# Performance work log

Hardware: AMD Instinct MI355X
Metric: run time of the kernel (lower is better)

Reference implementation:

```python
import jax, jax.numpy as jnp
import numpy as np
from math import ceil

B, T, FQ, D = 2, 48, 100, 512
H, DFF, L, WSZ = 8, 2048, 6, 8


def setup_inputs() -> dict:
    key = jax.random.key(0)
    ks = jax.random.split(key, 8)
    g = lambda k, shape: jax.random.normal(k, shape, jnp.float32) * 0.02
    return {
        "frame_queries": jax.random.normal(ks[0], (B, T, FQ, D), jnp.float32),
        "Wp": g(ks[1], (D, D)), "bp": jnp.zeros((D,), jnp.float32),
        "Wqkv": g(ks[2], (L, 3 * D, D)), "bqkv": jnp.zeros((L, 3 * D), jnp.float32),
        "Wo": g(ks[3], (L, D, D)), "bo": jnp.zeros((L, D), jnp.float32),
        "ln1_s": jnp.ones((L, D), jnp.float32), "ln1_b": jnp.zeros((L, D), jnp.float32),
        "W1": g(ks[4], (L, DFF, D)), "b1": jnp.zeros((L, DFF), jnp.float32),
        "W2": g(ks[5], (L, D, DFF)), "b2": jnp.zeros((L, D), jnp.float32),
        "ln2_s": jnp.ones((L, D), jnp.float32), "ln2_b": jnp.zeros((L, D), jnp.float32),
    }


def _ln(x, s, b, eps=1e-5):
    mu = x.mean(-1, keepdims=True)
    var = ((x - mu) ** 2).mean(-1, keepdims=True)
    return (x - mu) * jax.lax.rsqrt(var + eps) * s + b


def _mha(x, Wqkv_i, bqkv_i, Wo_i, bo_i, add_mask):
    # x: [Bw, S, C]; add_mask: None or [Bw, 1, S, S] additive float
    Bw, S, C = x.shape
    hd = C // H
    qkv = x @ Wqkv_i.T + bqkv_i
    q, k, v = jnp.split(qkv, 3, axis=-1)
    q = q.reshape(Bw, S, H, hd).transpose(0, 2, 1, 3)
    k = k.reshape(Bw, S, H, hd).transpose(0, 2, 1, 3)
    v = v.reshape(Bw, S, H, hd).transpose(0, 2, 1, 3)
    scores = jnp.einsum('bhqd,bhkd->bhqk', q, k) * jnp.float32(1.0 / np.sqrt(hd))
    if add_mask is not None:
        scores = scores + add_mask
    a = jax.nn.softmax(scores, axis=-1)
    o = jnp.einsum('bhqk,bhkd->bhqd', a, v).transpose(0, 2, 1, 3).reshape(Bw, S, C)
    return o @ Wo_i.T + bo_i


def _shift_mask():
    # padding mask is all-False (T % WSZ == 0), faithful construction of the
    # shifted-window additive mask as in the torch code.
    Nw = T // WSZ
    half = int(ceil(WSZ / 2))
    S = WSZ * FQ
    am = jnp.zeros((B, T), dtype=bool)
    r = jnp.roll(am, half, axis=1).reshape(B, Nw, WSZ)
    m = jnp.broadcast_to(r[..., None], (B, Nw, WSZ, WSZ))
    m = m.at[:, 0].set(m[:, 0] | m[:, 0].swapaxes(-1, -2))
    m = m.at[:, -1].set(m[:, -1] | m[:, -1].swapaxes(-1, -2))
    m = m.at[:, 0, :half, half:].set(True)
    m = m.at[:, 0, half:, :half].set(True)
    mfull = jnp.broadcast_to(m.reshape(B * Nw, WSZ, 1, WSZ, 1),
                             (B * Nw, WSZ, FQ, WSZ, FQ)).reshape(B * Nw, S, S)
    return (mfull.astype(jnp.float32) * -1000.0)[:, None]  # [B*Nw,1,S,S]


def reference(frame_queries, Wp, bp, Wqkv, bqkv, Wo, bo, ln1_s, ln1_b,
              W1, b1, W2, b2, ln2_s, ln2_b):
    Nw = T // WSZ
    half = int(ceil(WSZ / 2))
    S = WSZ * FQ
    x = frame_queries @ Wp.T + bp  # [B, T, FQ, D]
    shift_add = _shift_mask()
    for i in range(L):
        if i % 2 == 0:
            # plain window attention
            xw = x.reshape(B * Nw, S, D)
            xw = _ln(xw + _mha(xw, Wqkv[i], bqkv[i], Wo[i], bo[i], None),
                     ln1_s[i], ln1_b[i])
            x = xw.reshape(B, T, FQ, D)
        else:
            # shifted window attention
            xs = jnp.roll(x, half, axis=1)
            xw = xs.reshape(B * Nw, S, D)
            xw = _ln(xw + _mha(xw, Wqkv[i], bqkv[i], Wo[i], bo[i], shift_add),
                     ln1_s[i], ln1_b[i])
            x = jnp.roll(xw.reshape(B, T, FQ, D), -half, axis=1)
        # FFN (pointwise over channel dim)
        h = jax.nn.relu(x @ W1[i].T + b1[i]) @ W2[i].T + b2[i]
        x = _ln(x + h, ln2_s[i], ln2_b[i])
    return x  # [B, T, FQ, D] == 'lb t nq c'
```

## Files before the change

### kernel.cpp

```cpp
#include <hip/hip_runtime.h>


typedef float  f4    __attribute__((ext_vector_type(4)));
typedef __bf16 bf8   __attribute__((ext_vector_type(8)));
typedef unsigned short u16x8 __attribute__((ext_vector_type(8)));
typedef unsigned short u16x4 __attribute__((ext_vector_type(4)));

__device__ __forceinline__ unsigned short f2bf(float f) {
    unsigned int u = __builtin_bit_cast(unsigned int, f);
    u += 0x7fffu + ((u >> 16) & 1u);
    return (unsigned short)(u >> 16);
}
__device__ __forceinline__ float bf2f(unsigned short s) {
    return __builtin_bit_cast(float, ((unsigned int)s) << 16);
}

#define GLD16(gp, lp) __builtin_amdgcn_global_load_lds( \
    (const __attribute__((address_space(1))) void*)(gp), \
    (__attribute__((address_space(3))) void*)(lp), 16, 0, 0)

__device__ __forceinline__ int map_row(int r, int rshift) {
    if (!rshift) return r;
    int bb = r / 4800, rem = r % 4800;
    int tt = rem / 100, f = rem - tt * 100;
    return bb * 4800 + ((tt + rshift) % 48) * 100 + f;
}

template<int BM>
__global__ __launch_bounds__(256) void mfma_gemm(
    const unsigned short* __restrict__ A, const unsigned short* __restrict__ W,
    const float* __restrict__ bias, float* Cf, unsigned short* Cb,
    int M, int N, int K, int relu, int rshift, int qscale, int NB, int nsplit)
{
    constexpr int MI      = BM / 32;
    constexpr int ABUF    = BM * 32;
    constexpr int SB      = ABUF + 4096;
    constexpr int AROUNDS = BM / 64;
    __shared__ unsigned short Ls[3 * SB];
    const int tid = threadIdx.x, lane = tid & 63, wave = tid >> 6;

    const int per = gridDim.x >> 3;
    const int l = (blockIdx.x & 7) * per + (blockIdx.x >> 3);
    const int MB = M / BM;
    if (l >= NB * MB * nsplit) return;
    const int sk = l / (NB * MB);
    const int l2 = l - sk * NB * MB;
    const int n0 = (l2 % NB) * 128, m0 = (l2 / NB) * BM;
    const int Ksp = K / nsplit;
    const int kbeg = sk * Ksp;

    const unsigned short* ga[AROUNDS];
    #pragma unroll
    for (int it = 0; it < AROUNDS; ++it) {
        int s = it * 256 + tid, row = s >> 2, cg = (s & 3) ^ ((row >> 1) & 3);
        ga[it] = A + (size_t)map_row(m0 + row, rshift) * K + kbeg + cg * 8;
    }
    const unsigned short* gb[2];
    #pragma unroll
    for (int it = 0; it < 2; ++it) {
        int s = it * 256 + tid, row = s >> 2, cg = (s & 3) ^ ((row >> 1) & 3);
        gb[it] = W + (size_t)(n0 + row) * K + kbeg + cg * 8;
    }

    const int wm = (wave >> 1) * (BM / 2), wn = (wave & 1) * 64;
    const int lr = lane & 15, quad = lane >> 4;

    auto STAGE = [&](int kt2, int buf) {
        const int k1 = kt2 << 5;
        unsigned short* Lb = &Ls[buf * SB];
        #pragma unroll
        for (int it = 0; it < AROUNDS; ++it)
            GLD16(ga[it] + k1, &Lb[(it * 256 + wave * 64) * 8]);
        #pragma unroll
        for (int it = 0; it < 2; ++it)
            GLD16(gb[it] + k1, &Lb[ABUF + (it * 256 + wave * 64) * 8]);
    };

    f4 acc[MI][4];
    #pragma unroll
    for (int i = 0; i < MI; ++i)
        #pragma unroll
        for (int j = 0; j < 4; ++j) acc[i][j] = 0.f;

    const int NK = Ksp >> 5;
    STAGE(0, 0);
    STAGE(1, 1);

    int cb = 0;
    for (int kt = 0; kt < NK; ++kt) {
        if (kt + 1 < NK) {
            if constexpr (BM == 128) asm volatile("s_waitcnt vmcnt(4)" ::: "memory");
            else                     asm volatile("s_waitcnt vmcnt(3)" ::: "memory");
        } else {
            asm volatile("s_waitcnt vmcnt(0)" ::: "memory");
        }
        __builtin_amdgcn_s_barrier();
        __builtin_amdgcn_sched_barrier(0);
        const int ib = (cb == 0) ? 2 : cb - 1;
        if (kt + 2 < NK) STAGE(kt + 2, ib);

        const unsigned short* Ab = &Ls[cb * SB];
        const unsigned short* Bb = &Ls[cb * SB + ABUF];
        bf8 af[MI], bfr[4];
        #pragma unroll
        for (int mi = 0; mi < MI; ++mi) {
            int m = wm + mi * 16 + lr;
            int c = quad ^ ((m >> 1) & 3);
            af[mi] = __builtin_bit_cast(bf8, *(const u16x8*)&Ab[(m * 4 + c) * 8]);
        }
        #pragma unroll
        for (int ni = 0; ni < 4; ++ni) {
            int n = wn + ni * 16 + lr;
            int c = quad ^ ((n >> 1) & 3);
            bfr[ni] = __builtin_bit_cast(bf8, *(const u16x8*)&Bb[(n * 4 + c) * 8]);
        }
        #pragma unroll
        for (int mi = 0; mi < MI; ++mi)
            #pragma unroll
            for (int ni = 0; ni < 4; ++ni)
                acc[mi][ni] = __builtin_amdgcn_mfma_f32_16x16x32_bf16(
                    af[mi], bfr[ni], acc[mi][ni], 0, 0, 0);
        __builtin_amdgcn_sched_barrier(0);
        cb = (cb + 1 == 3) ? 0 : cb + 1;
    }

    float* Cfo = Cf ? Cf + (size_t)sk * M * N : nullptr;
    unsigned short* Cbo = Cb ? Cb + (size_t)sk * M * N : nullptr;
    #pragma unroll
    for (int mi = 0; mi < MI; ++mi) {
        #pragma unroll
        for (int ni = 0; ni < 4; ++ni) {
            const int rowg = m0 + wm + mi * 16 + quad * 4;
            const int colg = n0 + wn + ni * 16 + lr;
            const float bv = (sk == 0) ? bias[colg] : 0.f;
            const float sc = (qscale && colg < 512) ? 0.125f : 1.0f;
            #pragma unroll
            for (int r = 0; r < 4; ++r) {
                float v = (acc[mi][ni][r] + bv) * sc;
                if (relu) v = fmaxf(v, 0.f);
                const size_t off = (size_t)(rowg + r) * N + colg;
                if (Cfo) Cfo[off] = v;
                if (Cbo) Cbo[off] = f2bf(v);
            }
        }
    }
}

__global__ __launch_bounds__(320) void flash_attn_mfma(
    const unsigned short* __restrict__ qkv, unsigned short* __restrict__ o,
    int masked)
{
    __shared__ unsigned short Ks[2][2048];
    __shared__ unsigned short VT[2][64 * 34];
    __shared__ unsigned short Ps[5][576];

    const int bid = blockIdx.x;
    const int h = bid & 7, kk2 = bid >> 3;
    const int qt = kk2 % 10, w = kk2 / 10;
    const int tid = threadIdx.x, lane = tid & 63, wave = tid >> 6;
    const int lr = lane & 15, quad = lane >> 4;
    const int qb = qt * 80 + wave * 16;
    const size_t wbase = (size_t)w * 800 * 1536;
    const bool do_mask = masked && ((w % 6) == 0);

    bf8 aQ[2];
    {
        const unsigned short* qp =
            qkv + wbase + (size_t)(qb + lr) * 1536 + h * 64 + quad * 8;
        aQ[0] = __builtin_bit_cast(bf8, *(const u16x8*)qp);
        aQ[1] = __builtin_bit_cast(bf8, *(const u16x8*)(qp + 32));
    }

    const unsigned short* gk = qkv;
    int kw = 0;
    if (wave < 4) {
        int s = wave * 64 + lane, row = s >> 3, clog = (s & 7) ^ (row & 7);
        gk = qkv + wbase + (size_t)row * 1536 + 512 + h * 64 + clog * 8;
        kw = wave * 512;
    }
    const int vkey = tid >> 3, vd0 = (tid & 7) * 8;
    const unsigned short* gv =
        qkv + wbase + (size_t)vkey * 1536 + 1024 + h * 64 + vd0;

    float lsum = 0.f;
    f4 oacc[4];
    #pragma unroll
    for (int dt = 0; dt < 4; ++dt) oacc[dt] = 0.f;

    const bool qhl = (qb + lr) >= 400;

    if (wave < 4) GLD16(gk, &Ks[0][kw]);
    if (tid < 256) {
        u16x8 vv0 = *(const u16x8*)gv;
        #pragma unroll
        for (int j = 0; j < 8; ++j) VT[0][(vd0 + j) * 34 + vkey] = vv0[j];
    }

    for (int kt = 0; kt < 25; ++kt) {
        const int cb = kt & 1, nb = cb ^ 1;
        const int k0 = kt * 32;
        __syncthreads();

        u16x8 vv;
        const bool pf = (kt < 24);
        if (pf && wave < 4) GLD16(gk + (size_t)(k0 + 32) * 1536, &Ks[nb][kw]);
        if (pf && tid < 256) vv = *(const u16x8*)(gv + (size_t)(k0 + 32) * 1536);

        f4 st[2];
        st[0] = 0.f; st[1] = 0.f;
        #pragma unroll
        for (int kh = 0; kh < 2; ++kh) {
            const int cx = (kh * 4 + quad) ^ (lane & 7);
            bf8 kf0 = __builtin_bit_cast(bf8, *(const u16x8*)&Ks[cb][(lr * 8 + cx) * 8]);
            bf8 kf1 = __builtin_bit_cast(bf8, *(const u16x8*)&Ks[cb][((16 + lr) * 8 + cx) * 8]);
            st[0] = __builtin_amdgcn_mfma_f32_16x16x32_bf16(kf0, aQ[kh], st[0], 0, 0, 0);
            st[1] = __builtin_amdgcn_mfma_f32_16x16x32_bf16(kf1, aQ[kh], st[1], 0, 0, 0);
        }

        {
            u16x4 pk0, pk1;
            float ls = 0.f;
            #pragma unroll
            for (int r = 0; r < 4; ++r) {
                float a = st[0][r], b = st[1][r];
                if (do_mask) {
                    if (((k0 + quad * 4 + r) >= 400) != qhl)      a -= 1000.f;
                    if (((k0 + 16 + quad * 4 + r) >= 400) != qhl) b -= 1000.f;
                }
                float p0 = __expf(fminf(a, 80.f));
                float p1 = __expf(fminf(b, 80.f));
                ls += p0 + p1;
                pk0[r] = (unsigned short)(__builtin_bit_cast(unsigned int, p0) >> 16);
                pk1[r] = (unsigned short)(__builtin_bit_cast(unsigned int, p1) >> 16);
            }
            lsum += ls;
            *(u16x4*)&Ps[wave][lr * 36 + quad * 4]      = pk0;
            *(u16x4*)&Ps[wave][lr * 36 + 16 + quad * 4] = pk1;
        }

        if (pf && tid < 256) {
            #pragma unroll
            for (int j = 0; j < 8; ++j) VT[nb][(vd0 + j) * 34 + vkey] = vv[j];
        }

        bf8 aP = __builtin_bit_cast(bf8, *(const u16x8*)&Ps[wave][lr * 36 + quad * 8]);
        #pragma unroll
        for (int dt = 0; dt < 4; ++dt) {
            bf8 bV = __builtin_bit_cast(bf8,
                *(const u16x8*)&VT[cb][(dt * 16 + lr) * 34 + quad * 8]);
            oacc[dt] = __builtin_amdgcn_mfma_f32_16x16x32_bf16(aP, bV, oacc[dt], 0, 0, 0);
        }
    }

    {
        float l = lsum;
        l += __shfl_xor(l, 16);
        l += __shfl_xor(l, 32);
        float inv[4];
        #pragma unroll
        for (int r = 0; r < 4; ++r)
            inv[r] = 1.0f / __shfl(l, quad * 4 + r);
        #pragma unroll
        for (int dt = 0; dt < 4; ++dt)
            #pragma unroll
            for (int r = 0; r < 4; ++r)
                o[((size_t)w * 800 + qb + quad * 4 + r) * 512 + h * 64 + dt * 16 + lr] =
                    f2bf(oacc[dt][r] * inv[r]);
    }
}

__global__ __launch_bounds__(256) void add_ln_kernel(
    const unsigned short* xb, const unsigned short* dlt,
    const unsigned short* dlt2,
    const float* __restrict__ s, const float* __restrict__ b,
    float* outf, unsigned short* outb, int rshift)
{
    const int wave = threadIdx.x >> 6, lane = threadIdx.x & 63;
    const int row = blockIdx.x * 4 + wave;
    const int xrow = map_row(row, rshift);
    const int c = lane * 8;
    u16x8 xv = *(const u16x8*)(xb  + (size_t)xrow * 512 + c);
    u16x8 dv = *(const u16x8*)(dlt + (size_t)row  * 512 + c);
    u16x8 dv2 = {0,0,0,0,0,0,0,0};
    if (dlt2) dv2 = *(const u16x8*)(dlt2 + (size_t)row * 512 + c);
    f4 u0, u1;
    #pragma unroll
    for (int j = 0; j < 4; ++j) {
        u0[j] = bf2f(xv[j])     + bf2f(dv[j]);
        u1[j] = bf2f(xv[4 + j]) + bf2f(dv[4 + j]);
        if (dlt2) { u0[j] += bf2f(dv2[j]); u1[j] += bf2f(dv2[4 + j]); }
    }
    float sum = u0[0]+u0[1]+u0[2]+u0[3] + u1[0]+u1[1]+u1[2]+u1[3];
    #pragma unroll
    for (int o2 = 1; o2 < 64; o2 <<= 1) sum += __shfl_xor(sum, o2);
    const float mu = sum * (1.0f / 512.0f);
    f4 d0 = u0 - mu, d1 = u1 - mu;
    float sq = d0[0]*d0[0]+d0[1]*d0[1]+d0[2]*d0[2]+d0[3]*d0[3]
             + d1[0]*d1[0]+d1[1]*d1[1]+d1[2]*d1[2]+d1[3]*d1[3];
    #pragma unroll
    for (int o2 = 1; o2 < 64; o2 <<= 1) sq += __shfl_xor(sq, o2);
    const float rs = rsqrtf(sq * (1.0f / 512.0f) + 1e-5f);
    f4 s0 = *(const f4*)(s + c), s1 = *(const f4*)(s + c + 4);
    f4 b0 = *(const f4*)(b + c), b1 = *(const f4*)(b + c + 4);
    f4 y0, y1;
    #pragma unroll
    for (int j = 0; j < 4; ++j) { y0[j] = d0[j]*rs*s0[j]+b0[j]; y1[j] = d1[j]*rs*s1[j]+b1[j]; }
    u16x8 ob;
    #pragma unroll
    for (int j = 0; j < 4; ++j) { ob[j] = f2bf(y0[j]); ob[4+j] = f2bf(y1[j]); }
    *(u16x8*)(outb + (size_t)xrow * 512 + c) = ob;
    if (outf) {
        float* of = outf + (size_t)xrow * 512 + c;
        *(f4*)of = y0; *(f4*)(of + 4) = y1;
    }
}

__global__ __launch_bounds__(256) void cast_f2b_kernel(
    const float* __restrict__ in, unsigned short* __restrict__ out, int n4)
{
    const int i = blockIdx.x * 256 + threadIdx.x;
    if (i >= n4) return;
    f4 v = ((const f4*)in)[i];
    u16x4 o4 = {f2bf(v[0]), f2bf(v[1]), f2bf(v[2]), f2bf(v[3])};
    ((u16x4*)out)[i] = o4;
}

extern "C" void kernel_launch(void* const* d_in, const int* in_sizes, int n_in,
                              void* d_out, int out_size, void* d_ws, size_t ws_size,
                              hipStream_t stream)
{
    const float* fq   = (const float*)d_in[0];
    const float* Wp   = (const float*)d_in[1];
    const float* bp   = (const float*)d_in[2];
    const float* Wqkv = (const float*)d_in[3];
    const float* bqkv = (const float*)d_in[4];
    const float* Wo   = (const float*)d_in[5];
    const float* bo   = (const float*)d_in[6];
    const float* l1s  = (const float*)d_in[7];
    const float* l1b  = (const float*)d_in[8];
    const float* W1   = (const float*)d_in[9];
    const float* b1   = (const float*)d_in[10];
    const float* W2   = (const float*)d_in[11];
    const float* b2   = (const float*)d_in[12];
    const float* l2s  = (const float*)d_in[13];
    const float* l2b  = (const float*)d_in[14];
    float* out = (float*)d_out;

    unsigned short* xb   = (unsigned short*)d_ws;
    unsigned short* qkvb = xb + 4915200;
    unsigned short* hbuf = qkvb + 14745600;
    unsigned short* wbuf = hbuf + 19660800;
    unsigned short* obuf = hbuf;
    unsigned short* t1b  = qkvb;
    unsigned short* t1b2 = qkvb + 4915200;
    unsigned short* fqb  = hbuf;
    unsigned short* wqA = wbuf;
    unsigned short* woA = wqA + 4718592;
    unsigned short* w1A = woA + 1572864;
    unsigned short* w2A = w1A + 6291456;
    unsigned short* wpA = w2A + 6291456;

    const dim3 blk(256);
    #define G8(n) dim3((((n) + 7) & ~7))
    cast_f2b_kernel<<<dim3(4800), blk, 0, stream>>>(fq,   fqb, 1228800);
    cast_f2b_kernel<<<dim3(4608), blk, 0, stream>>>(Wqkv, wqA, 1179648);
    cast_f2b_kernel<<<dim3(1536), blk, 0, stream>>>(Wo,   woA, 393216);
    cast_f2b_kernel<<<dim3(6144), blk, 0, stream>>>(W1,   w1A, 1572864);
    cast_f2b_kernel<<<dim3(6144), blk, 0, stream>>>(W2,   w2A, 1572864);
    cast_f2b_kernel<<<dim3(256),  blk, 0, stream>>>(Wp,   wpA, 65536);
    mfma_gemm<64><<<G8(600), blk, 0, stream>>>(fqb, wpA, bp, nullptr, xb,
                                               9600, 512, 512, 0, 0, 0, 4, 1);

    for (int i = 0; i < 6; ++i) {
        const int rsh = (i & 1) ? 44 : 0;
        const unsigned short* wq = wqA + (size_t)i * 786432;
        const unsigned short* wo = woA + (size_t)i * 262144;
        const unsigned short* w1 = w1A + (size_t)i * 1048576;
        const unsigned short* w2 = w2A + (size_t)i * 1048576;
        mfma_gemm<128><<<G8(900), blk, 0, stream>>>(xb, wq, bqkv + i * 1536,
                                                    nullptr, qkvb, 9600, 1536, 512, 0, rsh, 1, 12, 1);
        flash_attn_mfma<<<dim3(960), dim3(320), 0, stream>>>(qkvb, obuf, i & 1);
        mfma_gemm<128><<<G8(600), blk, 0, stream>>>(obuf, wo, bo + i * 512,
                                                    nullptr, t1b, 9600, 512, 512, 0, 0, 0, 4, 2);
        add_ln_kernel<<<dim3(2400), blk, 0, stream>>>(xb, t1b, t1b2, l1s + i * 512, l1b + i * 512,
                                                      nullptr, xb, rsh);
        mfma_gemm<128><<<G8(1200), blk, 0, stream>>>(xb, w1, b1 + i * 2048,
                                                     nullptr, hbuf, 9600, 2048, 512, 1, 0, 0, 16, 1);
        mfma_gemm<128><<<G8(600), blk, 0, stream>>>(hbuf, w2, b2 + i * 512,
                                                    nullptr, t1b, 9600, 512, 2048, 0, 0, 0, 4, 2);
        add_ln_kernel<<<dim3(2400), blk, 0, stream>>>(xb, t1b, t1b2, l2s + i * 512, l2b + i * 512,
                                                      (i == 5) ? out : nullptr, xb, 0);
    }
    #undef G8
}
```

Before: 1.252 ms.

## Widen attention key tiles to 64 and drop split-K in output GEMMs

The flash attention kernel now processes 64 keys per iteration instead of 32, running 13 iterations with the last half-tile zeroed. This halves the barrier and prefetch count per block and doubles the MFMA work between syncs, with s_setprio raised around the MFMA sections. The Wo and W2 projections switch from a 128-tile split-K of 2 to a 64-tile GEMM without split-K, so add_ln no longer has to sum two partial buffers. The cost is more LDS per attention block, which may lower occupancy, and smaller tiles in the N=512 GEMMs.

```diff
diff --git a/kernel.cpp b/kernel.cpp
--- a/kernel.cpp
+++ b/kernel.cpp
@@ -150,9 +150,9 @@
     const unsigned short* __restrict__ qkv, unsigned short* __restrict__ o,
     int masked)
 {
-    __shared__ unsigned short Ks[2][2048];
-    __shared__ unsigned short VT[2][64 * 34];
-    __shared__ unsigned short Ps[5][576];
+    __shared__ unsigned short Ks[2][4096];
+    __shared__ unsigned short VT[2][64 * 66];
+    __shared__ unsigned short Ps[5][16 * 68];
 
     const int bid = blockIdx.x;
     const int h = bid & 7, kk2 = bid >> 3;
@@ -171,16 +171,19 @@
         aQ[1] = __builtin_bit_cast(bf8, *(const u16x8*)(qp + 32));
     }
 
-    const unsigned short* gk = qkv;
-    int kw = 0;
+    const unsigned short* gkc[2] = {qkv, qkv};
+    int krow[2] = {0, 0};
     if (wave < 4) {
-        int s = wave * 64 + lane, row = s >> 3, clog = (s & 7) ^ (row & 7);
-        gk = qkv + wbase + (size_t)row * 1536 + 512 + h * 64 + clog * 8;
-        kw = wave * 512;
+        #pragma unroll
+        for (int t = 0; t < 2; ++t) {
+            int s = t * 256 + wave * 64 + lane;
+            int row = s >> 3, cg = (s & 7) ^ (row & 7);
+            krow[t] = row;
+            gkc[t] = qkv + wbase + 512 + h * 64 + cg * 8;
+        }
     }
     const int vkey = tid >> 3, vd0 = (tid & 7) * 8;
-    const unsigned short* gv =
-        qkv + wbase + (size_t)vkey * 1536 + 1024 + h * 64 + vd0;
+    const unsigned short* gvb = qkv + wbase + 1024 + h * 64 + vd0;
 
     float lsum = 0.f;
     f4 oacc[4];
@@ -189,67 +192,99 @@
 
     const bool qhl = (qb + lr) >= 400;
 
-    if (wave < 4) GLD16(gk, &Ks[0][kw]);
+    if (wave < 4) {
+        GLD16(gkc[0] + (size_t)krow[0] * 1536, &Ks[0][(wave * 64) * 8]);
+        GLD16(gkc[1] + (size_t)krow[1] * 1536, &Ks[0][(256 + wave * 64) * 8]);
+    }
     if (tid < 256) {
-        u16x8 vv0 = *(const u16x8*)gv;
-        #pragma unroll
-        for (int j = 0; j < 8; ++j) VT[0][(vd0 + j) * 34 + vkey] = vv0[j];
-    }
-
-    for (int kt = 0; kt < 25; ++kt) {
+        #pragma unroll
+        for (int t = 0; t < 2; ++t) {
+            u16x8 vv0 = *(const u16x8*)(gvb + (size_t)(vkey + t * 32) * 1536);
+            #pragma unroll
+            for (int j = 0; j < 8; ++j) VT[0][(vd0 + j) * 66 + vkey + t * 32] = vv0[j];
+        }
+    }
+
+    for (int kt = 0; kt < 13; ++kt) {
         const int cb = kt & 1, nb = cb ^ 1;
-        const int k0 = kt * 32;
+        const int k0 = kt * 64;
         __syncthreads();
 
-        u16x8 vv;
-        const bool pf = (kt < 24);
-        if (pf && wave < 4) GLD16(gk + (size_t)(k0 + 32) * 1536, &Ks[nb][kw]);
-        if (pf && tid < 256) vv = *(const u16x8*)(gv + (size_t)(k0 + 32) * 1536);
-
-        f4 st[2];
-        st[0] = 0.f; st[1] = 0.f;
+        const bool pf = (kt < 12);
+        if (pf && wave < 4) {
+            #pragma unroll
+            for (int t = 0; t < 2; ++t) {
+                int r = k0 + 64 + krow[t]; if (r > 799) r = 799;
+                GLD16(gkc[t] + (size_t)r * 1536, &Ks[nb][(t * 256 + wave * 64) * 8]);
+            }
+        }
+        u16x8 vv[2];
+        if (pf && tid < 256) {
+            #pragma unroll
+            for (int t = 0; t < 2; ++t) {
+                int r = k0 + 64 + vkey + t * 32; if (r > 799) r = 799;
+                vv[t] = *(const u16x8*)(gvb + (size_t)r * 1536);
+            }
+        }
+
+        f4 st[4];
+        st[0] = 0.f; st[1] = 0.f; st[2] = 0.f; st[3] = 0.f;
+        __builtin_amdgcn_s_setprio(1);
         #pragma unroll
         for (int kh = 0; kh < 2; ++kh) {
             const int cx = (kh * 4 + quad) ^ (lane & 7);
-            bf8 kf0 = __builtin_bit_cast(bf8, *(const u16x8*)&Ks[cb][(lr * 8 + cx) * 8]);
-            bf8 kf1 = __builtin_bit_cast(bf8, *(const u16x8*)&Ks[cb][((16 + lr) * 8 + cx) * 8]);
-            st[0] = __builtin_amdgcn_mfma_f32_16x16x32_bf16(kf0, aQ[kh], st[0], 0, 0, 0);
-            st[1] = __builtin_amdgcn_mfma_f32_16x16x32_bf16(kf1, aQ[kh], st[1], 0, 0, 0);
-        }
+            #pragma unroll
+            for (int g = 0; g < 4; ++g) {
+                bf8 kf = __builtin_bit_cast(bf8,
+                    *(const u16x8*)&Ks[cb][((g * 16 + lr) * 8 + cx) * 8]);
+                st[g] = __builtin_amdgcn_mfma_f32_16x16x32_bf16(kf, aQ[kh], st[g], 0, 0, 0);
+            }
+        }
+        __builtin_amdgcn_s_setprio(0);
 
         {
-            u16x4 pk0, pk1;
             float ls = 0.f;
             #pragma unroll
-            for (int r = 0; r < 4; ++r) {
-                float a = st[0][r], b = st[1][r];
-                if (do_mask) {
-                    if (((k0 + quad * 4 + r) >= 400) != qhl)      a -= 1000.f;
-                    if (((k0 + 16 + quad * 4 + r) >= 400) != qhl) b -= 1000.f;
+            for (int g = 0; g < 4; ++g) {
+                const bool dead = (kt == 12) && (g >= 2);
+                u16x4 pk;
+                #pragma unroll
+                for (int r = 0; r < 4; ++r) {
+                    float a = st[g][r];
+                    if (do_mask) {
+                        if (((k0 + g * 16 + quad * 4 + r) >= 400) != qhl) a -= 1000.f;
+                    }
+                    float p = __expf(fminf(a, 80.f));
+                    if (dead) p = 0.f;
+                    ls += p;
+                    pk[r] = (unsigned short)(__builtin_bit_cast(unsigned int, p) >> 16);
                 }
-                float p0 = __expf(fminf(a, 80.f));
-                float p1 = __expf(fminf(b, 80.f));
-                ls += p0 + p1;
-                pk0[r] = (unsigned short)(__builtin_bit_cast(unsigned int, p0) >> 16);
-                pk1[r] = (unsigned short)(__builtin_bit_cast(unsigned int, p1) >> 16);
+                *(u16x4*)&Ps[wave][lr * 68 + g * 16 + quad * 4] = pk;
             }
             lsum += ls;
-            *(u16x4*)&Ps[wave][lr * 36 + quad * 4]      = pk0;
-            *(u16x4*)&Ps[wave][lr * 36 + 16 + quad * 4] = pk1;
         }
 
         if (pf && tid < 256) {
             #pragma unroll
-            for (int j = 0; j < 8; ++j) VT[nb][(vd0 + j) * 34 + vkey] = vv[j];
-        }
-
-        bf8 aP = __builtin_bit_cast(bf8, *(const u16x8*)&Ps[wave][lr * 36 + quad * 8]);
+            for (int t = 0; t < 2; ++t)
+                #pragma unroll
+                for (int j = 0; j < 8; ++j)
+                    VT[nb][(vd0 + j) * 66 + vkey + t * 32] = vv[t][j];
+        }
+
+        bf8 aP0 = __builtin_bit_cast(bf8, *(const u16x8*)&Ps[wave][lr * 68 + quad * 8]);
+        bf8 aP1 = __builtin_bit_cast(bf8, *(const u16x8*)&Ps[wave][lr * 68 + 32 + quad * 8]);
+        __builtin_amdgcn_s_setprio(1);
         #pragma unroll
         for (int dt = 0; dt < 4; ++dt) {
-            bf8 bV = __builtin_bit_cast(bf8,
-                *(const u16x8*)&VT[cb][(dt * 16 + lr) * 34 + quad * 8]);
-            oacc[dt] = __builtin_amdgcn_mfma_f32_16x16x32_bf16(aP, bV, oacc[dt], 0, 0, 0);
-        }
+            bf8 bV0 = __builtin_bit_cast(bf8,
+                *(const u16x8*)&VT[cb][(dt * 16 + lr) * 66 + quad * 8]);
+            bf8 bV1 = __builtin_bit_cast(bf8,
+                *(const u16x8*)&VT[cb][(dt * 16 + lr) * 66 + 32 + quad * 8]);
+            oacc[dt] = __builtin_amdgcn_mfma_f32_16x16x32_bf16(aP0, bV0, oacc[dt], 0, 0, 0);
+            oacc[dt] = __builtin_amdgcn_mfma_f32_16x16x32_bf16(aP1, bV1, oacc[dt], 0, 0, 0);
+        }
+        __builtin_amdgcn_s_setprio(0);
     }
 
     {
@@ -352,7 +387,6 @@
     unsigned short* wbuf = hbuf + 19660800;
     unsigned short* obuf = hbuf;
     unsigned short* t1b  = qkvb;
-    unsigned short* t1b2 = qkvb + 4915200;
     unsigned short* fqb  = hbuf;
     unsigned short* wqA = wbuf;
     unsigned short* woA = wqA + 4718592;
@@ -380,15 +414,15 @@
         mfma_gemm<128><<<G8(900), blk, 0, stream>>>(xb, wq, bqkv + i * 1536,
                                                     nullptr, qkvb, 9600, 1536, 512, 0, rsh, 1, 12, 1);
         flash_attn_mfma<<<dim3(960), dim3(320), 0, stream>>>(qkvb, obuf, i & 1);
-        mfma_gemm<128><<<G8(600), blk, 0, stream>>>(obuf, wo, bo + i * 512,
-                                                    nullptr, t1b, 9600, 512, 512, 0, 0, 0, 4, 2);
-        add_ln_kernel<<<dim3(2400), blk, 0, stream>>>(xb, t1b, t1b2, l1s + i * 512, l1b + i * 512,
+        mfma_gemm<64><<<G8(600), blk, 0, stream>>>(obuf, wo, bo + i * 512,
+                                                   nullptr, t1b, 9600, 512, 512, 0, 0, 0, 4, 1);
+        add_ln_kernel<<<dim3(2400), blk, 0, stream>>>(xb, t1b, nullptr, l1s + i * 512, l1b + i * 512,
                                                       nullptr, xb, rsh);
         mfma_gemm<128><<<G8(1200), blk, 0, stream>>>(xb, w1, b1 + i * 2048,
                                                      nullptr, hbuf, 9600, 2048, 512, 1, 0, 0, 16, 1);
-        mfma_gemm<128><<<G8(600), blk, 0, stream>>>(hbuf, w2, b2 + i * 512,
-                                                    nullptr, t1b, 9600, 512, 2048, 0, 0, 0, 4, 2);
-        add_ln_kernel<<<dim3(2400), blk, 0, stream>>>(xb, t1b, t1b2, l2s + i * 512, l2b + i * 512,
+        mfma_gemm<64><<<G8(600), blk, 0, stream>>>(hbuf, w2, b2 + i * 512,
+                                                   nullptr, t1b, 9600, 512, 2048, 0, 0, 0, 4, 1);
+        add_ln_kernel<<<dim3(2400), blk, 0, stream>>>(xb, t1b, nullptr, l2s + i * 512, l2b + i * 512,
                                                       (i == 5) ? out : nullptr, xb, 0);
     }
     #undef G8
```

New measurement: 1.359 ms. +8.6%, slower.
